# Performance work log

Hardware: AMD Instinct MI355X
Metric: run time of the kernel (lower is better)

Reference implementation:

```python
import jax, jax.numpy as jnp
import numpy as np

B, N, E, H = 16, 1024, 128, 8  # batch, num_patches, emb_dim, num_heads
INNER = E * H                   # inner_dim = emb_dim * num_heads = 1024
LN_EPS = 1e-5
NEG_MAX = jnp.finfo(jnp.float32).max  # module uses -finfo.max on the diagonal


def setup_inputs() -> dict:
    key = jax.random.key(0)
    k0, k1, k2 = jax.random.split(key, 3)
    x = jax.random.normal(k0, (B, N, E), dtype=jnp.float32)
    ln_w = jnp.ones((E,), jnp.float32)
    ln_b = jnp.zeros((E,), jnp.float32)
    w_qkv = jax.random.normal(k1, (E, 3 * INNER), jnp.float32) * (E ** -0.5)
    scale = jnp.full((H,), E ** -0.5, jnp.float32)  # learnable per-head LSA scale
    w_proj = jax.random.normal(k2, (INNER, E), jnp.float32) * (INNER ** -0.5)
    b_proj = jnp.zeros((E,), jnp.float32)
    return {"x": x, "ln_w": ln_w, "ln_b": ln_b, "w_qkv": w_qkv,
            "scale": scale, "w_proj": w_proj, "b_proj": b_proj}


def reference(x, ln_w, ln_b, w_qkv, scale, w_proj, b_proj):
    # LayerNorm over emb_dim
    mu = jnp.mean(x, axis=-1, keepdims=True)
    var = jnp.mean(jnp.square(x - mu), axis=-1, keepdims=True)
    xn = (x - mu) * jax.lax.rsqrt(var + LN_EPS) * ln_w + ln_b

    # QKV projection (no bias), chunk into q,k,v of [B,N,INNER]
    qkv = xn @ w_qkv
    q, k, v = jnp.split(qkv, 3, axis=-1)

    # 'b n (h d) -> b h n d' with h = H, d = E
    def to_heads(t):
        return t.reshape(B, N, H, E).transpose(0, 2, 1, 3)
    q, k, v = to_heads(q), to_heads(k), to_heads(v)

    # per-head learnable scale (LSA), then mask diagonal to -max
    dots = jnp.einsum("bhnd,bhmd->bhnm", q, k) * scale[None, :, None, None]
    idx = jnp.arange(N)
    dots = dots.at[:, :, idx, idx].set(-NEG_MAX)

    attn = jax.nn.softmax(dots, axis=-1)  # dropout p=0.0 -> identity
    out = jnp.einsum("bhnm,bhmd->bhnd", attn, v)

    # 'b h n d -> b n (h d)', then output projection (with bias)
    out = out.transpose(0, 2, 1, 3).reshape(B, N, INNER)
    return out @ w_proj + b_proj
```

## Files before the change

kernel.cpp:

```cpp
#include <hip/hip_runtime.h>
#include <hip/hip_bf16.h>

typedef __bf16 bf16x8 __attribute__((ext_vector_type(8)));
typedef _Float16 f16x4 __attribute__((ext_vector_type(4)));
typedef float f32x4 __attribute__((ext_vector_type(4)));

__device__ __forceinline__ unsigned short f2bf(float f) {
  union { __hip_bfloat16 h; unsigned short u; } cv;
  cv.h = __float2bfloat16(f);
  return cv.u;
}
__device__ __forceinline__ unsigned short f2h(float f) {
  union { _Float16 h; unsigned short u; } cv;
  cv.h = (_Float16)f;
  return cv.u;
}

__device__ __forceinline__ bf16x8 ld_frag(const unsigned short* p) {
  bf16x8 v;
  __builtin_memcpy(&v, __builtin_assume_aligned(p, 16), 16);
  return v;
}
__device__ __forceinline__ f16x4 ld_h4(const unsigned short* p) {
  f16x4 v;
  __builtin_memcpy(&v, __builtin_assume_aligned(p, 8), 8);
  return v;
}
__device__ __forceinline__ uint4 ld16(const unsigned short* p) {
  uint4 v;
  __builtin_memcpy(&v, __builtin_assume_aligned(p, 16), 16);
  return v;
}
__device__ __forceinline__ void st16(unsigned short* p, uint4 v) {
  __builtin_memcpy(__builtin_assume_aligned(p, 16), &v, 16);
}
__device__ __forceinline__ void dma16(const unsigned short* g, unsigned short* l) {
  __builtin_amdgcn_global_load_lds((const __attribute__((address_space(1))) void*)g,
                                   (__attribute__((address_space(3))) void*)l, 16, 0, 0);
}

__global__ __launch_bounds__(256) void prolog_kernel(const float* __restrict__ x,
                                                     const float* __restrict__ lw,
                                                     const float* __restrict__ lb,
                                                     const float* __restrict__ w_qkv,
                                                     const float* __restrict__ w_proj,
                                                     unsigned short* __restrict__ xn,
                                                     unsigned short* __restrict__ wqkvT,
                                                     unsigned short* __restrict__ wprojT) {
  __shared__ float tile[32][33];
  int idx = blockIdx.x;
  if (idx < 4096) {
    int wave = threadIdx.x >> 6;
    int lane = threadIdx.x & 63;
    int row = idx * 4 + wave;
    const float* xr = x + (size_t)row * 128;
    float2 v = *reinterpret_cast<const float2*>(xr + lane * 2);
    float s1 = v.x + v.y;
    float s2 = v.x * v.x + v.y * v.y;
#pragma unroll
    for (int off = 32; off > 0; off >>= 1) {
      s1 += __shfl_xor(s1, off, 64);
      s2 += __shfl_xor(s2, off, 64);
    }
    float mu = s1 * (1.0f / 128.0f);
    float var = s2 * (1.0f / 128.0f) - mu * mu;
    float rstd = rsqrtf(var + 1e-5f);
    float a0 = (v.x - mu) * rstd * lw[lane * 2] + lb[lane * 2];
    float a1 = (v.y - mu) * rstd * lw[lane * 2 + 1] + lb[lane * 2 + 1];
    unsigned int pk = (unsigned int)f2bf(a0) | ((unsigned int)f2bf(a1) << 16);
    *reinterpret_cast<unsigned int*>(xn + (size_t)row * 128 + lane * 2) = pk;
    return;
  }
  const float* in;
  unsigned short* out;
  int R, C, cb, rb;
  if (idx < 4480) {
    int rem = idx - 4096;
    in = w_qkv; out = wqkvT; R = 128; C = 3072;
    cb = rem % 96; rb = rem / 96;
  } else {
    int rem = idx - 4480;
    in = w_proj; out = wprojT; R = 1024; C = 128;
    cb = rem % 4; rb = rem / 4;
  }
  int tx = threadIdx.x & 31, ty = threadIdx.x >> 5;
  int c0 = cb * 32, r0 = rb * 32;
#pragma unroll
  for (int k = 0; k < 4; k++)
    tile[ty + 8 * k][tx] = in[(size_t)(r0 + ty + 8 * k) * C + c0 + tx];
  __syncthreads();
#pragma unroll
  for (int k = 0; k < 4; k++)
    out[(size_t)(c0 + ty + 8 * k) * R + r0 + tx] = f2bf(tile[tx][ty + 8 * k]);
}

__global__ __launch_bounds__(256) void qkv_gemm(const unsigned short* __restrict__ A,
                                                const unsigned short* __restrict__ Bt,
                                                const float* __restrict__ scale,
                                                unsigned short* __restrict__ qk,
                                                unsigned short* __restrict__ Vt) {
  __shared__ unsigned short Al[128 * 72];
  __shared__ unsigned short Bl[128 * 72];
  int t = threadIdx.x;
  int i0 = blockIdx.x * 128, c0 = blockIdx.y * 128;
  int lg = t & 7, rr = t >> 3;
  int w = t >> 6, lane = t & 63, l15 = lane & 15, quad = lane >> 4;
  int wy = (w >> 1) * 64, wx = (w & 1) * 64;
  const f32x4 fz = {0.f, 0.f, 0.f, 0.f};
  f32x4 acc[4][4];
#pragma unroll
  for (int i = 0; i < 4; i++)
#pragma unroll
    for (int j = 0; j < 4; j++) acc[i][j] = fz;
  bool qkblk = (blockIdx.y < 16);

#pragma unroll
  for (int kt = 0; kt < 2; kt++) {
    int k0 = kt * 64;
    uint4 areg[4], breg[4];
#pragma unroll
    for (int p = 0; p < 4; p++)
      areg[p] = ld16(&A[(size_t)(i0 + rr + 32 * p) * 128 + k0 + lg * 8]);
#pragma unroll
    for (int p = 0; p < 4; p++)
      breg[p] = ld16(&Bt[(size_t)(c0 + rr + 32 * p) * 128 + k0 + lg * 8]);
    __syncthreads();
#pragma unroll
    for (int p = 0; p < 4; p++) st16(&Al[(rr + 32 * p) * 72 + lg * 8], areg[p]);
#pragma unroll
    for (int p = 0; p < 4; p++) st16(&Bl[(rr + 32 * p) * 72 + lg * 8], breg[p]);
    __syncthreads();
#pragma unroll
    for (int ks = 0; ks < 2; ks++) {
      bf16x8 af[4], bfr[4];
#pragma unroll
      for (int i = 0; i < 4; i++)
        af[i] = ld_frag(&Al[(wy + 16 * i + l15) * 72 + 32 * ks + quad * 8]);
#pragma unroll
      for (int j = 0; j < 4; j++)
        bfr[j] = ld_frag(&Bl[(wx + 16 * j + l15) * 72 + 32 * ks + quad * 8]);
      if (qkblk) {
#pragma unroll
        for (int i = 0; i < 4; i++)
#pragma unroll
          for (int j = 0; j < 4; j++)
            acc[i][j] = __builtin_amdgcn_mfma_f32_16x16x32_bf16(bfr[j], af[i], acc[i][j], 0, 0, 0);
      } else {
#pragma unroll
        for (int i = 0; i < 4; i++)
#pragma unroll
          for (int j = 0; j < 4; j++)
            acc[i][j] = __builtin_amdgcn_mfma_f32_16x16x32_bf16(af[i], bfr[j], acc[i][j], 0, 0, 0);
      }
    }
  }
  if (qkblk) {
    float qsc = (blockIdx.y < 8) ? scale[blockIdx.y] * 1.44269504f : 1.0f;
#pragma unroll
    for (int i = 0; i < 4; i++)
#pragma unroll
      for (int j = 0; j < 4; j++) {
        int row = i0 + wy + 16 * i + l15;
        int col = c0 + wx + 16 * j + quad * 4;
        ushort4 pk;
        pk.x = f2bf(acc[i][j][0] * qsc); pk.y = f2bf(acc[i][j][1] * qsc);
        pk.z = f2bf(acc[i][j][2] * qsc); pk.w = f2bf(acc[i][j][3] * qsc);
        *reinterpret_cast<ushort4*>(qk + (size_t)row * 2048 + col) = pk;
      }
  } else {
    int vc0 = (blockIdx.y - 16) * 128;
#pragma unroll
    for (int i = 0; i < 4; i++)
#pragma unroll
      for (int j = 0; j < 4; j++) {
        int vcol = vc0 + wx + 16 * j + l15;
        int hh = vcol >> 7, dd = vcol & 127;
        int row0 = i0 + wy + 16 * i + quad * 4;
        int bb = row0 >> 10, nn = row0 & 1023;
        ushort4 pk;
        pk.x = f2h(acc[i][j][0]); pk.y = f2h(acc[i][j][1]);
        pk.z = f2h(acc[i][j][2]); pk.w = f2h(acc[i][j][3]);
        *reinterpret_cast<ushort4*>(Vt + (size_t)(bb * 8 + hh) * 131072 +
                                    (size_t)dd * 1024 + nn) = pk;
      }
  }
}

__global__ __launch_bounds__(256, 2) void attn_kernel(const unsigned short* __restrict__ qk,
                                                      const unsigned short* __restrict__ Vt,
                                                      unsigned short* __restrict__ aout) {
  __shared__ __align__(16) unsigned short Kl[2][64 * 128];
  __shared__ __align__(16) unsigned short Vl[2][128 * 64];
  int t = threadIdx.x;
  int idx = blockIdx.x;
  int bh = idx & 127, qt = idx >> 7;
  int b = bh >> 3, h = bh & 7;
  int q0 = qt * 128;
  int w = t >> 6, lane = t & 63, l15 = lane & 15, quad = lane >> 4;

  bf16x8 qf[2][4];
  {
    const unsigned short* qb = qk + (size_t)(b * 1024) * 2048 + h * 128;
#pragma unroll
    for (int g = 0; g < 2; g++) {
      const unsigned short* qp = qb + (size_t)(q0 + 32 * w + 16 * g + l15) * 2048;
#pragma unroll
      for (int ks = 0; ks < 4; ks++) qf[g][ks] = ld_frag(qp + 32 * ks + quad * 8);
    }
  }
  const f32x4 fz = {0.f, 0.f, 0.f, 0.f};
  f32x4 o[2][8];
#pragma unroll
  for (int g = 0; g < 2; g++)
#pragma unroll
    for (int i = 0; i < 8; i++) o[g][i] = fz;
  float plsum[2] = {0.f, 0.f};

  const unsigned short* kbase = qk + (size_t)(b * 1024) * 2048 + 1024 + h * 128;
  const unsigned short* vbase = Vt + (size_t)bh * 131072;

  int koff[4], voff[4];
#pragma unroll
  for (int i = 0; i < 4; i++) {
    int c = w * 4 + i;
    int krow = c * 4 + (lane >> 4);
    int kg = ((lane & 15) ^ (krow & 7)) * 8;
    koff[i] = krow * 2048 + kg;
    int vrow = c * 8 + (lane >> 3);
    int vg = ((lane & 7) ^ ((vrow >> 1) & 7)) * 8;
    voff[i] = vrow * 1024 + vg;
  }

#pragma unroll
  for (int i = 0; i < 4; i++) {
    dma16(kbase + koff[i], &Kl[0][(w * 4 + i) * 512]);
    dma16(vbase + voff[i], &Vl[0][(w * 4 + i) * 512]);
  }

  for (int kt = 0; kt < 16; kt++) {
    int k0 = kt * 64;
    __syncthreads();
    {
      int nb = (kt + 1) & 1;
      int kn0 = ((kt + 1) & 15) * 64;
#pragma unroll
      for (int i = 0; i < 4; i++) {
        dma16(kbase + (size_t)kn0 * 2048 + koff[i], &Kl[nb][(w * 4 + i) * 512]);
        dma16(vbase + voff[i] + kn0, &Vl[nb][(w * 4 + i) * 512]);
      }
    }
    const unsigned short* Kc = Kl[kt & 1];
    const unsigned short* Vc = Vl[kt & 1];

#pragma unroll
    for (int ct = 0; ct < 4; ct++) {
      f32x4 acc[2] = {fz, fz};
#pragma unroll
      for (int ks = 0; ks < 4; ks++) {
        bf16x8 kf = ld_frag(&Kc[(16 * ct + l15) * 128 + ((4 * ks + quad) ^ (l15 & 7)) * 8]);
#pragma unroll
        for (int g = 0; g < 2; g++)
          acc[g] = __builtin_amdgcn_mfma_f32_16x16x32_bf16(kf, qf[g][ks], acc[g], 0, 0, 0);
      }
      f16x4 pa[2];
#pragma unroll
      for (int g = 0; g < 2; g++) {
        if ((q0 + 32 * w + 16 * g) == (k0 + 16 * ct)) {
#pragma unroll
          for (int r = 0; r < 4; r++) {
            float p = ((quad * 4 + r) == l15) ? 0.f : exp2f(acc[g][r]);
            plsum[g] += p;
            pa[g][r] = (_Float16)p;
          }
        } else {
#pragma unroll
          for (int r = 0; r < 4; r++) {
            float p = exp2f(acc[g][r]);
            plsum[g] += p;
            pa[g][r] = (_Float16)p;
          }
        }
      }
#pragma unroll
      for (int c8 = 0; c8 < 8; c8++) {
        f16x4 vf = ld_h4(&Vc[(16 * c8 + l15) * 64 + ((4 * ct + quad) ^ (l15 & 14)) * 4]);
#pragma unroll
        for (int g = 0; g < 2; g++)
          o[g][c8] = __builtin_amdgcn_mfma_f32_16x16x16f16(pa[g], vf, o[g][c8], 0, 0, 0);
      }
    }
  }

#pragma unroll
  for (int g = 0; g < 2; g++) {
    float s = plsum[g];
    s += __shfl_xor(s, 16, 64);
    s += __shfl_xor(s, 32, 64);
#pragma unroll
    for (int r = 0; r < 4; r++) {
      float rs = __shfl(s, (lane & 48) + quad * 4 + r, 64);
      float rl = 1.0f / rs;
      int row = b * 1024 + q0 + 32 * w + 16 * g + quad * 4 + r;
#pragma unroll
      for (int c8 = 0; c8 < 8; c8++) {
        int col = h * 128 + 16 * c8 + l15;
        aout[(size_t)row * 1024 + col] = f2bf(o[g][c8][r] * rl);
      }
    }
  }
}

__global__ __launch_bounds__(256) void proj_gemm(const unsigned short* __restrict__ A,
                                                 const unsigned short* __restrict__ Bt,
                                                 const float* __restrict__ bias,
                                                 float* __restrict__ out) {
  __shared__ unsigned short Al[64 * 136];
  __shared__ unsigned short Bl[64 * 136];
  int t = threadIdx.x;
  int i0 = blockIdx.x * 64, c0 = blockIdx.y * 64;
  int w = t >> 6, lane = t & 63, l15 = lane & 15, quad = lane >> 4;
  int wy = (w >> 1) * 32, wx = (w & 1) * 32;
  const f32x4 fz = {0.f, 0.f, 0.f, 0.f};
  f32x4 acc[2][2];
#pragma unroll
  for (int i = 0; i < 2; i++)
#pragma unroll
    for (int j = 0; j < 2; j++) acc[i][j] = fz;
  int l = t & 15, rr = t >> 4;
  for (int kb = 0; kb < 8; kb++) {
    int k0 = kb * 128;
    uint4 areg[4], breg[4];
#pragma unroll
    for (int p = 0; p < 4; p++)
      areg[p] = ld16(&A[(size_t)(i0 + rr + 16 * p) * 1024 + k0 + l * 8]);
#pragma unroll
    for (int p = 0; p < 4; p++)
      breg[p] = ld16(&Bt[(size_t)(c0 + rr + 16 * p) * 1024 + k0 + l * 8]);
    __syncthreads();
#pragma unroll
    for (int p = 0; p < 4; p++) st16(&Al[(rr + 16 * p) * 136 + l * 8], areg[p]);
#pragma unroll
    for (int p = 0; p < 4; p++) st16(&Bl[(rr + 16 * p) * 136 + l * 8], breg[p]);
    __syncthreads();
#pragma unroll
    for (int ks = 0; ks < 4; ks++) {
      bf16x8 af[2], bfr[2];
#pragma unroll
      for (int i = 0; i < 2; i++)
        af[i] = ld_frag(&Al[(wy + 16 * i + l15) * 136 + 32 * ks + quad * 8]);
#pragma unroll
      for (int j = 0; j < 2; j++)
        bfr[j] = ld_frag(&Bl[(wx + 16 * j + l15) * 136 + 32 * ks + quad * 8]);
#pragma unroll
      for (int i = 0; i < 2; i++)
#pragma unroll
        for (int j = 0; j < 2; j++)
          acc[i][j] = __builtin_amdgcn_mfma_f32_16x16x32_bf16(af[i], bfr[j], acc[i][j], 0, 0, 0);
    }
  }
#pragma unroll
  for (int i = 0; i < 2; i++)
#pragma unroll
    for (int j = 0; j < 2; j++) {
      int col = c0 + wx + 16 * j + l15;
      float bv = bias[col];
#pragma unroll
      for (int r = 0; r < 4; r++) {
        int row = i0 + wy + 16 * i + quad * 4 + r;
        out[(size_t)row * 128 + col] = acc[i][j][r] + bv;
      }
    }
}

extern "C" void kernel_launch(void* const* d_in, const int* in_sizes, int n_in,
                              void* d_out, int out_size, void* d_ws, size_t ws_size,
                              hipStream_t stream) {
  const float* x      = (const float*)d_in[0];
  const float* ln_w   = (const float*)d_in[1];
  const float* ln_b   = (const float*)d_in[2];
  const float* w_qkv  = (const float*)d_in[3];
  const float* scale  = (const float*)d_in[4];
  const float* w_proj = (const float*)d_in[5];
  const float* b_proj = (const float*)d_in[6];
  float* out = (float*)d_out;

  char* ws = (char*)d_ws;
  unsigned short* xn     = (unsigned short*)(ws);
  unsigned short* wqkvT  = (unsigned short*)(ws + 4194304);
  unsigned short* wprojT = (unsigned short*)(ws + 4980736);
  unsigned short* qk     = (unsigned short*)(ws + 5242880);
  unsigned short* Vt     = (unsigned short*)(ws + 72351744);
  unsigned short* aout   = (unsigned short*)(ws + 105906176);

  prolog_kernel<<<dim3(4608), dim3(256), 0, stream>>>(x, ln_w, ln_b, w_qkv, w_proj,
                                                      xn, wqkvT, wprojT);
  qkv_gemm<<<dim3(128, 24), dim3(256), 0, stream>>>(xn, wqkvT, scale, qk, Vt);
  attn_kernel<<<dim3(1024), dim3(256), 0, stream>>>(qk, Vt, aout);
  proj_gemm<<<dim3(256, 2), dim3(256), 0, stream>>>(aout, wprojT, b_proj, out);
}
```

Measured before the change: 220.6 us.

## Fuse output projection into attention epilogue with atomic accumulation

Removes the separate projection GEMM. Each attention block multiplies its normalized per-head output tile by the matching slice of the projection weights and accumulates into the fp32 output with atomicAdd; a small kernel pre-fills the output with the bias. This avoids writing and re-reading the intermediate attention output and one launch. In exchange it adds many global atomics and a nondeterministic summation order. The softmax exponent also switches from exp2 with a folded log2e scale to __expf.

New measurement: 237.1 us. 1.08x slower.

```diff
diff --git a/kernel.cpp b/kernel.cpp
--- a/kernel.cpp
+++ b/kernel.cpp
@@ -94,6 +94,13 @@
     out[(size_t)(c0 + ty + 8 * k) * R + r0 + tx] = f2bf(tile[tx][ty + 8 * k]);
 }
 
+__global__ __launch_bounds__(256) void bias_init(const float* __restrict__ bias,
+                                                 float* __restrict__ out) {
+  int i = blockIdx.x * 256 + threadIdx.x;
+  float4 bv = *reinterpret_cast<const float4*>(bias + (i & 31) * 4);
+  reinterpret_cast<float4*>(out)[i] = bv;
+}
+
 __global__ __launch_bounds__(256) void qkv_gemm(const unsigned short* __restrict__ A,
                                                 const unsigned short* __restrict__ Bt,
                                                 const float* __restrict__ scale,
@@ -155,7 +162,7 @@
     }
   }
   if (qkblk) {
-    float qsc = (blockIdx.y < 8) ? scale[blockIdx.y] * 1.44269504f : 1.0f;
+    float qsc = (blockIdx.y < 8) ? scale[blockIdx.y] : 1.0f;
 #pragma unroll
     for (int i = 0; i < 4; i++)
 #pragma unroll
@@ -188,9 +195,11 @@
 
 __global__ __launch_bounds__(256, 2) void attn_kernel(const unsigned short* __restrict__ qk,
                                                       const unsigned short* __restrict__ Vt,
-                                                      unsigned short* __restrict__ aout) {
-  __shared__ __align__(16) unsigned short Kl[2][64 * 128];
-  __shared__ __align__(16) unsigned short Vl[2][128 * 64];
+                                                      const unsigned short* __restrict__ wprojT,
+                                                      float* __restrict__ out) {
+  __shared__ __align__(16) unsigned short smem[32768];
+  unsigned short* KlB = smem;
+  unsigned short* VlB = smem + 16384;
   int t = threadIdx.x;
   int idx = blockIdx.x;
   int bh = idx & 127, qt = idx >> 7;
@@ -233,24 +242,24 @@
 
 #pragma unroll
   for (int i = 0; i < 4; i++) {
-    dma16(kbase + koff[i], &Kl[0][(w * 4 + i) * 512]);
-    dma16(vbase + voff[i], &Vl[0][(w * 4 + i) * 512]);
+    dma16(kbase + koff[i], &KlB[(w * 4 + i) * 512]);
+    dma16(vbase + voff[i], &VlB[(w * 4 + i) * 512]);
   }
 
   for (int kt = 0; kt < 16; kt++) {
     int k0 = kt * 64;
     __syncthreads();
-    {
+    if (kt < 15) {
       int nb = (kt + 1) & 1;
-      int kn0 = ((kt + 1) & 15) * 64;
+      int kn0 = (kt + 1) * 64;
 #pragma unroll
       for (int i = 0; i < 4; i++) {
-        dma16(kbase + (size_t)kn0 * 2048 + koff[i], &Kl[nb][(w * 4 + i) * 512]);
-        dma16(vbase + voff[i] + kn0, &Vl[nb][(w * 4 + i) * 512]);
-      }
-    }
-    const unsigned short* Kc = Kl[kt & 1];
-    const unsigned short* Vc = Vl[kt & 1];
+        dma16(kbase + (size_t)kn0 * 2048 + koff[i], &KlB[nb * 8192 + (w * 4 + i) * 512]);
+        dma16(vbase + voff[i] + kn0, &VlB[nb * 8192 + (w * 4 + i) * 512]);
+      }
+    }
+    const unsigned short* Kc = KlB + (kt & 1) * 8192;
+    const unsigned short* Vc = VlB + (kt & 1) * 8192;
 
 #pragma unroll
     for (int ct = 0; ct < 4; ct++) {
@@ -268,14 +277,14 @@
         if ((q0 + 32 * w + 16 * g) == (k0 + 16 * ct)) {
 #pragma unroll
           for (int r = 0; r < 4; r++) {
-            float p = ((quad * 4 + r) == l15) ? 0.f : exp2f(acc[g][r]);
+            float p = ((quad * 4 + r) == l15) ? 0.f : __expf(acc[g][r]);
             plsum[g] += p;
             pa[g][r] = (_Float16)p;
           }
         } else {
 #pragma unroll
           for (int r = 0; r < 4; r++) {
-            float p = exp2f(acc[g][r]);
+            float p = __expf(acc[g][r]);
             plsum[g] += p;
             pa[g][r] = (_Float16)p;
           }
@@ -291,85 +300,53 @@
     }
   }
 
+  float rl[2][4];
 #pragma unroll
   for (int g = 0; g < 2; g++) {
     float s = plsum[g];
     s += __shfl_xor(s, 16, 64);
     s += __shfl_xor(s, 32, 64);
 #pragma unroll
-    for (int r = 0; r < 4; r++) {
-      float rs = __shfl(s, (lane & 48) + quad * 4 + r, 64);
-      float rl = 1.0f / rs;
-      int row = b * 1024 + q0 + 32 * w + 16 * g + quad * 4 + r;
-#pragma unroll
-      for (int c8 = 0; c8 < 8; c8++) {
-        int col = h * 128 + 16 * c8 + l15;
-        aout[(size_t)row * 1024 + col] = f2bf(o[g][c8][r] * rl);
-      }
-    }
-  }
-}
-
-__global__ __launch_bounds__(256) void proj_gemm(const unsigned short* __restrict__ A,
-                                                 const unsigned short* __restrict__ Bt,
-                                                 const float* __restrict__ bias,
-                                                 float* __restrict__ out) {
-  __shared__ unsigned short Al[64 * 136];
-  __shared__ unsigned short Bl[64 * 136];
-  int t = threadIdx.x;
-  int i0 = blockIdx.x * 64, c0 = blockIdx.y * 64;
-  int w = t >> 6, lane = t & 63, l15 = lane & 15, quad = lane >> 4;
-  int wy = (w >> 1) * 32, wx = (w & 1) * 32;
-  const f32x4 fz = {0.f, 0.f, 0.f, 0.f};
-  f32x4 acc[2][2];
-#pragma unroll
-  for (int i = 0; i < 2; i++)
-#pragma unroll
-    for (int j = 0; j < 2; j++) acc[i][j] = fz;
-  int l = t & 15, rr = t >> 4;
-  for (int kb = 0; kb < 8; kb++) {
-    int k0 = kb * 128;
-    uint4 areg[4], breg[4];
-#pragma unroll
-    for (int p = 0; p < 4; p++)
-      areg[p] = ld16(&A[(size_t)(i0 + rr + 16 * p) * 1024 + k0 + l * 8]);
-#pragma unroll
-    for (int p = 0; p < 4; p++)
-      breg[p] = ld16(&Bt[(size_t)(c0 + rr + 16 * p) * 1024 + k0 + l * 8]);
-    __syncthreads();
-#pragma unroll
-    for (int p = 0; p < 4; p++) st16(&Al[(rr + 16 * p) * 136 + l * 8], areg[p]);
-#pragma unroll
-    for (int p = 0; p < 4; p++) st16(&Bl[(rr + 16 * p) * 136 + l * 8], breg[p]);
-    __syncthreads();
-#pragma unroll
-    for (int ks = 0; ks < 4; ks++) {
-      bf16x8 af[2], bfr[2];
-#pragma unroll
-      for (int i = 0; i < 2; i++)
-        af[i] = ld_frag(&Al[(wy + 16 * i + l15) * 136 + 32 * ks + quad * 8]);
-#pragma unroll
-      for (int j = 0; j < 2; j++)
-        bfr[j] = ld_frag(&Bl[(wx + 16 * j + l15) * 136 + 32 * ks + quad * 8]);
-#pragma unroll
-      for (int i = 0; i < 2; i++)
-#pragma unroll
-        for (int j = 0; j < 2; j++)
-          acc[i][j] = __builtin_amdgcn_mfma_f32_16x16x32_bf16(af[i], bfr[j], acc[i][j], 0, 0, 0);
-    }
-  }
-#pragma unroll
-  for (int i = 0; i < 2; i++)
-#pragma unroll
-    for (int j = 0; j < 2; j++) {
-      int col = c0 + wx + 16 * j + l15;
-      float bv = bias[col];
-#pragma unroll
-      for (int r = 0; r < 4; r++) {
-        int row = i0 + wy + 16 * i + quad * 4 + r;
-        out[(size_t)row * 128 + col] = acc[i][j][r] + bv;
-      }
-    }
+    for (int r = 0; r < 4; r++)
+      rl[g][r] = 1.0f / __shfl(s, (lane & 48) + quad * 4 + r, 64);
+  }
+  __syncthreads();
+  unsigned short* Tl = smem;
+#pragma unroll
+  for (int g = 0; g < 2; g++)
+#pragma unroll
+    for (int c8 = 0; c8 < 8; c8++)
+#pragma unroll
+      for (int r = 0; r < 4; r++)
+        Tl[(32 * w + 16 * g + quad * 4 + r) * 136 + 16 * c8 + l15] =
+            f2bf(o[g][c8][r] * rl[g][r]);
+  __syncthreads();
+
+  bf16x8 af[2][4];
+#pragma unroll
+  for (int gg = 0; gg < 2; gg++)
+#pragma unroll
+    for (int ks = 0; ks < 4; ks++)
+      af[gg][ks] = ld_frag(&Tl[(32 * w + 16 * gg + l15) * 136 + 32 * ks + quad * 8]);
+  const unsigned short* wp = wprojT;
+  size_t orow0 = (size_t)(b * 1024 + q0 + 32 * w);
+#pragma unroll
+  for (int jt = 0; jt < 8; jt++) {
+    bf16x8 bfr[4];
+#pragma unroll
+    for (int ks = 0; ks < 4; ks++)
+      bfr[ks] = ld_frag(&wp[(size_t)(16 * jt + l15) * 1024 + h * 128 + 32 * ks + quad * 8]);
+#pragma unroll
+    for (int gg = 0; gg < 2; gg++) {
+      f32x4 acc = fz;
+#pragma unroll
+      for (int ks = 0; ks < 4; ks++)
+        acc = __builtin_amdgcn_mfma_f32_16x16x32_bf16(af[gg][ks], bfr[ks], acc, 0, 0, 0);
+#pragma unroll
+      for (int r = 0; r < 4; r++)
+        atomicAdd(&out[(orow0 + 16 * gg + quad * 4 + r) * 128 + 16 * jt + l15], acc[r]);
+    }
+  }
 }
 
 extern "C" void kernel_launch(void* const* d_in, const int* in_sizes, int n_in,
@@ -390,11 +367,10 @@
   unsigned short* wprojT = (unsigned short*)(ws + 4980736);
   unsigned short* qk     = (unsigned short*)(ws + 5242880);
   unsigned short* Vt     = (unsigned short*)(ws + 72351744);
-  unsigned short* aout   = (unsigned short*)(ws + 105906176);
 
   prolog_kernel<<<dim3(4608), dim3(256), 0, stream>>>(x, ln_w, ln_b, w_qkv, w_proj,
                                                       xn, wqkvT, wprojT);
+  bias_init<<<dim3(2048), dim3(256), 0, stream>>>(b_proj, out);
   qkv_gemm<<<dim3(128, 24), dim3(256), 0, stream>>>(xn, wqkvT, scale, qk, Vt);
-  attn_kernel<<<dim3(1024), dim3(256), 0, stream>>>(qk, Vt, aout);
-  proj_gemm<<<dim3(256, 2), dim3(256), 0, stream>>>(aout, wprojT, b_proj, out);
-}
+  attn_kernel<<<dim3(1024), dim3(256), 0, stream>>>(qk, Vt, wprojT, out);
+}
```
